# Kernel optimization log

Hardware: AMD Instinct MI355X
Metric: run time of the kernel (lower is better)

The kernel has to match this reference:

```python
import jax, jax.numpy as jnp
import numpy as np

INF_SUB_NUM = -9000000000000000.0
LN_EPS = 1e-5


def _layernorm(x, gamma, beta):
    mu = jnp.mean(x, axis=-1, keepdims=True)
    var = jnp.mean(jnp.square(x - mu), axis=-1, keepdims=True)
    return gamma * (x - mu) * jax.lax.rsqrt(var + LN_EPS) + beta


def setup_inputs() -> dict:
    key = jax.random.key(0)
    kh, ke, kt, kw1, kw2 = jax.random.split(key, 5)
    B, N, E, D = 8, 4096, 2048, 256
    stdv = 1.0 / np.sqrt(D)
    return {
        "hidden": jax.random.normal(kh, (B, N, D), dtype=jnp.float32),
        "ht": jax.random.randint(kt, (B, E, N), 0, 2, dtype=jnp.int32),
        "edge_emb": jax.random.normal(ke, (B, E, D), dtype=jnp.float32),
        "wnk": jax.random.uniform(kw1, (D, D), jnp.float32, -stdv, stdv),
        "wek": jax.random.uniform(kw2, (D, D), jnp.float32, -stdv, stdv),
        "ln_gamma": jnp.ones((D,), jnp.float32),
        "ln_beta": jnp.zeros((D,), jnp.float32),
    }


def reference(hidden, ht, edge_emb, wnk, wek, ln_gamma, ln_beta):
    # hidden: [B,N,D]; ht: [B,E,N] incidence; edge_emb: [B,E,D]
    D = hidden.shape[-1]
    scale = 1.0 / jnp.sqrt(jnp.float32(D))

    edge_emb = _layernorm(edge_emb, ln_gamma, ln_beta)          # [B,E,D]
    node_k = hidden @ wnk                                        # [B,N,D]

    # Stage 1: edges attend over their incident nodes (softmax over N, dim=2)
    edge_scores = jnp.einsum('bed,bnd->ben', edge_emb, node_k) * scale
    edge_scores = jnp.where(ht > 0, edge_scores, INF_SUB_NUM)
    attn_edge = jax.nn.softmax(edge_scores, axis=2)              # [B,E,N]
    edge_h = jnp.einsum('ben,bnd->bed', attn_edge, hidden) + edge_emb

    # Stage 2: nodes gather from edges; softmax over N (dim=1), as in source
    edge_k = edge_h @ wek                                        # [B,E,D]
    node_scores = jnp.einsum('bnd,bed->bne', node_k, edge_k) * scale
    node_scores = jnp.where(jnp.transpose(ht, (0, 2, 1)) > 0, node_scores, INF_SUB_NUM)
    attn_node = jax.nn.softmax(node_scores, axis=1)              # [B,N,E]
    node_hidden = jnp.einsum('bne,bed->bnd', attn_node, edge_h)  # [B,N,D]
    return node_hidden
```

## Files before the change

### kernel.cpp

```cpp
#include <hip/hip_runtime.h>
#include <hip/hip_bf16.h>
#include <stdint.h>


#define B_ 8
#define N_ 4096
#define E_ 2048
#define D_ 256

typedef short bf16x8 __attribute__((ext_vector_type(8)));
typedef float f32x4 __attribute__((ext_vector_type(4)));
typedef unsigned short us8 __attribute__((ext_vector_type(8)));

#define AS1 __attribute__((address_space(1)))
#define AS3 __attribute__((address_space(3)))

__device__ __forceinline__ unsigned short f2bf(float f) {
    union { float f; unsigned int u; } v; v.f = f;
    unsigned int r = v.u + 0x7fffu + ((v.u >> 16) & 1u);
    return (unsigned short)(r >> 16);
}
__device__ __forceinline__ float bf2f(unsigned short h) {
    union { unsigned int u; float f; } v; v.u = ((unsigned int)h) << 16;
    return v.f;
}
__device__ __forceinline__ float waveReduceSum(float v) {
#pragma unroll
    for (int o = 32; o > 0; o >>= 1) v += __shfl_xor(v, o, 64);
    return v;
}

__global__ __launch_bounds__(256) void ln_kernel(const float* __restrict__ x,
                                                 const float* __restrict__ gamma,
                                                 const float* __restrict__ beta,
                                                 unsigned short* __restrict__ yb) {
    __shared__ float red[8];
    const int row = blockIdx.x;
    const int t = threadIdx.x;
    const int lane = t & 63, wid = t >> 6;
    const float v = x[(size_t)row * D_ + t];
    float s = waveReduceSum(v);
    if (lane == 0) red[wid] = s;
    __syncthreads();
    const float mu = (red[0] + red[1] + red[2] + red[3]) * (1.0f / D_);
    const float d = v - mu;
    float s2 = waveReduceSum(d * d);
    if (lane == 0) red[4 + wid] = s2;
    __syncthreads();
    const float var = (red[4] + red[5] + red[6] + red[7]) * (1.0f / D_);
    yb[(size_t)row * D_ + t] = f2bf(gamma[t] * d * rsqrtf(var + 1e-5f) + beta[t]);
}

__global__ __launch_bounds__(256) void pack_mask(const int* __restrict__ ht,
                                                 uint32_t* __restrict__ bits) {
    __shared__ __align__(8) unsigned char nib[256];
    const int row = blockIdx.x;
    const int t = threadIdx.x;
    const int* hrow = ht + (size_t)row * N_;
    uint32_t* brow = bits + (size_t)row * (N_ / 32);
#pragma unroll
    for (int it = 0; it < 4; ++it) {
        const int4 v = *(const int4*)&hrow[it * 1024 + t * 4];
        unsigned char n = (unsigned char)((v.x > 0) | ((v.y > 0) << 1) |
                                          ((v.z > 0) << 2) | ((v.w > 0) << 3));
        nib[t] = n;
        __syncthreads();
        if (t < 32) {
            uint64_t x = *(const uint64_t*)&nib[t * 8];
            x = (x | (x >> 4)) & 0x00FF00FF00FF00FFull;
            x = (x | (x >> 8)) & 0x0000FFFF0000FFFFull;
            brow[it * 32 + t] = (uint32_t)(x | (x >> 16));
        }
        __syncthreads();
    }
}

__global__ __launch_bounds__(256) void prep_hidden(const float* __restrict__ in,
                                                   unsigned short* __restrict__ hb,
                                                   unsigned short* __restrict__ hT) {
    __shared__ unsigned short tile[64][65];
    const int b = blockIdx.z;
    in += (size_t)b * N_ * D_;
    hb += (size_t)b * N_ * D_;
    hT += (size_t)b * D_ * N_;
    const int n0 = blockIdx.y * 64, d0 = blockIdx.x * 64;
    const int t = threadIdx.x;
    const int tr = t >> 4, tc = (t & 15) * 4;
#pragma unroll
    for (int q = 0; q < 4; ++q) {
        const int rr = q * 16 + tr;
        const float4 f = *(const float4*)&in[(size_t)(n0 + rr) * D_ + d0 + tc];
        unsigned short h0 = f2bf(f.x), h1 = f2bf(f.y), h2 = f2bf(f.z), h3 = f2bf(f.w);
        *(ushort4*)&hb[(size_t)(n0 + rr) * D_ + d0 + tc] = make_ushort4(h0, h1, h2, h3);
        tile[rr][tc + 0] = h0; tile[rr][tc + 1] = h1;
        tile[rr][tc + 2] = h2; tile[rr][tc + 3] = h3;
    }
    __syncthreads();
#pragma unroll
    for (int q = 0; q < 4; ++q) {
        const int cc = q * 16 + tr;
        ushort4 o = make_ushort4(tile[tc + 0][cc], tile[tc + 1][cc],
                                 tile[tc + 2][cc], tile[tc + 3][cc]);
        *(ushort4*)&hT[(size_t)(d0 + cc) * N_ + n0 + tc] = o;
    }
}

__global__ __launch_bounds__(256) void cast_wT(const float* __restrict__ w,
                                               unsigned short* __restrict__ wT) {
    const int gid = blockIdx.x * 256 + threadIdx.x;
    const int i = gid >> 8, j = gid & 255;
    wT[j * D_ + i] = f2bf(w[i * D_ + j]);
}

__global__ __launch_bounds__(256) void scale_ehT(const float* __restrict__ ehT,
                                                 const float* __restrict__ lsum,
                                                 unsigned short* __restrict__ ehs) {
    const size_t base = ((size_t)blockIdx.x * 256 + threadIdx.x) * 8;
    const int b = (int)(base / ((size_t)D_ * E_));
    const int e = (int)(base % E_);
    const float4 f0 = *(const float4*)&ehT[base];
    const float4 f1 = *(const float4*)&ehT[base + 4];
    const float4 l0 = *(const float4*)&lsum[(size_t)b * E_ + e];
    const float4 l1 = *(const float4*)&lsum[(size_t)b * E_ + e + 4];
    us8 o;
    o[0] = f2bf(f0.x / l0.x); o[1] = f2bf(f0.y / l0.y);
    o[2] = f2bf(f0.z / l0.z); o[3] = f2bf(f0.w / l0.w);
    o[4] = f2bf(f1.x / l1.x); o[5] = f2bf(f1.y / l1.y);
    o[6] = f2bf(f1.z / l1.z); o[7] = f2bf(f1.w / l1.w);
    *(us8*)&ehs[base] = o;
}

__global__ __launch_bounds__(256) void gemm_bf16(const short* __restrict__ A,
                                                 const short* __restrict__ Bm,
                                                 unsigned short* __restrict__ C) {
    __shared__ __align__(16) short ls[16896];
    short* lsA = ls;
    short* lsB = ls + 8192;
    const int m0 = blockIdx.y * 128, n0 = blockIdx.x * 128;
    const int tid = threadIdx.x, wid = tid >> 6, lane = tid & 63;
    const int l15 = lane & 15, kg = lane >> 4;
    const int wr = wid >> 1, wc = wid & 1;

    int raoff[4], rota[4], rboff[4], rotb[4];
#pragma unroll
    for (int i = 0; i < 4; ++i) {
        const int ra = wr * 64 + i * 16 + l15;
        raoff[i] = ra * 64; rota[i] = kg + (ra >> 1);
        const int rb = wc * 64 + i * 16 + l15;
        rboff[i] = rb * 64; rotb[i] = kg + (rb >> 1);
    }
    const f32x4 zero = {0.f, 0.f, 0.f, 0.f};
    f32x4 acc[4][4];
#pragma unroll
    for (int i = 0; i < 4; ++i)
#pragma unroll
        for (int j = 0; j < 4; ++j) acc[i][j] = zero;

    for (int kt = 0; kt < 256; kt += 64) {
        __syncthreads();
#pragma unroll
        for (int q = 0; q < 4; ++q) {
            const int c = q * 256 + tid;
            const int r = c >> 3;
            const int kc = ((c & 7) - (r >> 1)) & 7;
            const short* ga = A + (size_t)(m0 + r) * 256 + kt + kc * 8;
            __builtin_amdgcn_global_load_lds((const AS1 void*)ga,
                (AS3 void*)(lsA + (q * 256 + wid * 64) * 8), 16, 0, 0);
            const short* gb = Bm + (size_t)(n0 + r) * 256 + kt + kc * 8;
            __builtin_amdgcn_global_load_lds((const AS1 void*)gb,
                (AS3 void*)(lsB + (q * 256 + wid * 64) * 8), 16, 0, 0);
        }
        __syncthreads();
#pragma unroll
        for (int s = 0; s < 2; ++s) {
            bf16x8 fa[4], fb[4];
#pragma unroll
            for (int i = 0; i < 4; ++i)
                fa[i] = *(const bf16x8*)(lsA + raoff[i] + (((s * 4 + rota[i]) & 7) << 3));
#pragma unroll
            for (int j = 0; j < 4; ++j)
                fb[j] = *(const bf16x8*)(lsB + rboff[j] + (((s * 4 + rotb[j]) & 7) << 3));
#pragma unroll
            for (int i = 0; i < 4; ++i)
#pragma unroll
                for (int j = 0; j < 4; ++j)
                    acc[i][j] = __builtin_amdgcn_mfma_f32_16x16x32_bf16(fa[i], fb[j], acc[i][j], 0, 0, 0);
        }
    }
    __syncthreads();
#pragma unroll
    for (int i = 0; i < 4; ++i)
#pragma unroll
        for (int r = 0; r < 4; ++r) {
            const int rowfull = wr * 64 + i * 16 + kg * 4 + r;
#pragma unroll
            for (int j = 0; j < 4; ++j) {
                const int cl = wc * 64 + j * 16 + l15;
                ls[rowfull * 132 + cl] = (short)f2bf(acc[i][j][r]);
            }
        }
    __syncthreads();
#pragma unroll
    for (int si = 0; si < 8; ++si) {
        const int row = (tid >> 4) + si * 16;
        const int col = (tid & 15) * 8;
        us8 val = *(us8*)&ls[row * 132 + col];
        *(us8*)&C[(size_t)(m0 + row) * D_ + n0 + col] = val;
    }
}

template <int MODE>
__global__ __launch_bounds__(256, 1) void fused_attn(
        const short* __restrict__ A, const short* __restrict__ B1,
        const short* __restrict__ B2, const uint32_t* __restrict__ bits,
        const unsigned short* __restrict__ eln,
        void* __restrict__ out1, float* __restrict__ out2,
        int KN, float scale) {
    __shared__ __align__(16) short ls[(MODE == 0) ? 33024 : 69888];
    const int b = blockIdx.x;
    const int m0 = blockIdx.y * 64;
    const int MA = (MODE == 2) ? N_ : E_;
    const short* Ab = A + (size_t)b * MA * D_;
    const short* B1b = B1 + (size_t)b * KN * D_;
    const short* B2b = (MODE != 0) ? (B2 + (size_t)b * D_ * KN) : nullptr;
    const uint32_t* bb = bits + (size_t)b * E_ * (N_ / 32);

    const int tid = threadIdx.x, wid = tid >> 6, lane = tid & 63;
    const int l15 = lane & 15, kg = lane >> 4;
    const int wv = wid >> 1, ww = wid & 1;

    bf16x8 fa[2][8];
#pragma unroll
    for (int mf = 0; mf < 2; ++mf) {
        const size_t ar = (size_t)(m0 + wv * 32 + mf * 16 + l15) * D_;
#pragma unroll
        for (int kf = 0; kf < 8; ++kf)
            fa[mf][kf] = *(const bf16x8*)(Ab + ar + (kf * 4 + kg) * 8);
    }

    const f32x4 zero = {0.f, 0.f, 0.f, 0.f};
    f32x4 acco[2][8];
    if (MODE != 0) {
#pragma unroll
        for (int mf = 0; mf < 2; ++mf)
#pragma unroll
            for (int jf = 0; jf < 8; ++jf) acco[mf][jf] = zero;
    }
    float rs[2][4] = {{0.f, 0.f, 0.f, 0.f}, {0.f, 0.f, 0.f, 0.f}};

    short* Pp = ls + 65536;
    const int NT = KN / 64;

#define STAGE_T(db, tt) do {                                                   \
        const int kt_ = (tt) * 64;                                             \
        short* b1d_ = ls + (db) * 16384;                                       \
        _Pragma("unroll")                                                      \
        for (int q = 0; q < 8; ++q) {                                          \
            const int c_ = q * 256 + tid;                                      \
            const int r_ = c_ >> 5;                                            \
            const int ck_ = (c_ & 31) ^ (r_ & 31);                             \
            __builtin_amdgcn_global_load_lds(                                  \
                (const AS1 void*)(B1b + (size_t)(kt_ + r_) * D_ + ck_ * 8),    \
                (AS3 void*)(b1d_ + (q * 256 + wid * 64) * 8), 16, 0, 0);       \
        }                                                                      \
        if (MODE != 0) {                                                       \
            short* b2d_ = ls + 32768 + (db) * 16384;                           \
            _Pragma("unroll")                                                  \
            for (int q = 0; q < 8; ++q) {                                      \
                const int c_ = q * 256 + tid;                                  \
                const int r_ = c_ >> 3;                                        \
                const int ck_ = (c_ & 7) ^ ((r_ >> 1) & 7);                    \
                __builtin_amdgcn_global_load_lds(                              \
                    (const AS1 void*)(B2b + (size_t)r_ * KN + kt_ + ck_ * 8),  \
                    (AS3 void*)(b2d_ + (q * 256 + wid * 64) * 8), 16, 0, 0);   \
            }                                                                  \
        }                                                                      \
    } while (0)

    STAGE_T(0, 0);
    __syncthreads();

    int cur = 0;
    for (int t = 0; t < NT; ++t) {
        if (t + 1 < NT) STAGE_T(cur ^ 1, t + 1);
        const short* b1c = ls + cur * 16384;
        f32x4 accs[2][2];
        accs[0][0] = zero; accs[0][1] = zero; accs[1][0] = zero; accs[1][1] = zero;
        const int rb0 = ww * 32 + l15, rb1 = ww * 32 + 16 + l15;
        const int x0 = kg ^ (rb0 & 31), x1 = kg ^ (rb1 & 31);
#pragma unroll
        for (int kf = 0; kf < 8; ++kf) {
            const bf16x8 fb0 = *(const bf16x8*)(b1c + rb0 * 256 + ((kf * 4) ^ x0) * 8);
            const bf16x8 fb1 = *(const bf16x8*)(b1c + rb1 * 256 + ((kf * 4) ^ x1) * 8);
            accs[0][0] = __builtin_amdgcn_mfma_f32_16x16x32_bf16(fa[0][kf], fb0, accs[0][0], 0, 0, 0);
            accs[1][0] = __builtin_amdgcn_mfma_f32_16x16x32_bf16(fa[1][kf], fb0, accs[1][0], 0, 0, 0);
            accs[0][1] = __builtin_amdgcn_mfma_f32_16x16x32_bf16(fa[0][kf], fb1, accs[0][1], 0, 0, 0);
            accs[1][1] = __builtin_amdgcn_mfma_f32_16x16x32_bf16(fa[1][kf], fb1, accs[1][1], 0, 0, 0);
        }
        const int kt0 = t * 64;
        uint64_t mw[2][4];
        uint32_t cw[2];
        if (MODE <= 1) {
#pragma unroll
            for (int mf = 0; mf < 2; ++mf)
#pragma unroll
                for (int r = 0; r < 4; ++r) {
                    const int row = m0 + wv * 32 + mf * 16 + kg * 4 + r;
                    mw[mf][r] = *(const uint64_t*)&bb[(size_t)row * (N_ / 32) + (kt0 >> 5)];
                }
        } else {
#pragma unroll
            for (int jf = 0; jf < 2; ++jf) {
                const int col = kt0 + ww * 32 + jf * 16 + l15;
                cw[jf] = bb[(size_t)col * (N_ / 32) + ((m0 + wv * 32) >> 5)];
            }
        }
#pragma unroll
        for (int mf = 0; mf < 2; ++mf)
#pragma unroll
            for (int jf = 0; jf < 2; ++jf)
#pragma unroll
                for (int r = 0; r < 4; ++r) {
                    float v = accs[mf][jf][r] * scale;
                    uint32_t bit;
                    if (MODE <= 1)
                        bit = (uint32_t)(mw[mf][r] >> (ww * 32 + jf * 16 + l15)) & 1u;
                    else
                        bit = (cw[jf] >> (mf * 16 + kg * 4 + r)) & 1u;
                    v = bit ? __expf(v) : 0.f;
                    if (MODE <= 1) rs[mf][r] += v;
                    if (MODE != 0) {
                        const int prow = wv * 32 + mf * 16 + kg * 4 + r;
                        const int pcol = ww * 32 + jf * 16 + l15;
                        Pp[prow * 64 + (((pcol >> 3) ^ ((prow >> 1) & 7)) * 8) + (pcol & 7)] =
                            (short)f2bf(v);
                    }
                }
        if (MODE != 0) {
            __syncthreads();
            const short* b2c = ls + 32768 + cur * 16384;
            const int pr0 = wv * 32 + l15, pr1 = wv * 32 + 16 + l15;
            const int px0 = kg ^ ((pr0 >> 1) & 7), px1 = kg ^ ((pr1 >> 1) & 7);
#pragma unroll
            for (int kf2 = 0; kf2 < 2; ++kf2) {
                const bf16x8 pa0 = *(const bf16x8*)(Pp + pr0 * 64 + ((kf2 * 4) ^ px0) * 8);
                const bf16x8 pa1 = *(const bf16x8*)(Pp + pr1 * 64 + ((kf2 * 4) ^ px1) * 8);
#pragma unroll
                for (int jf = 0; jf < 8; ++jf) {
                    const int rh = ww * 128 + jf * 16 + l15;
                    const bf16x8 fbh = *(const bf16x8*)(b2c + rh * 64 +
                        (((kf2 * 4 + kg) ^ ((rh >> 1) & 7))) * 8);
                    acco[0][jf] = __builtin_amdgcn_mfma_f32_16x16x32_bf16(pa0, fbh, acco[0][jf], 0, 0, 0);
                    acco[1][jf] = __builtin_amdgcn_mfma_f32_16x16x32_bf16(pa1, fbh, acco[1][jf], 0, 0, 0);
                }
            }
        }
        __syncthreads();
        cur ^= 1;
    }
#undef STAGE_T

    if (MODE == 0) {
        float* rsx = (float*)(ls + 32768);
#pragma unroll
        for (int mf = 0; mf < 2; ++mf)
#pragma unroll
            for (int r = 0; r < 4; ++r) {
                float s = rs[mf][r];
                s += __shfl_xor(s, 1, 64); s += __shfl_xor(s, 2, 64);
                s += __shfl_xor(s, 4, 64); s += __shfl_xor(s, 8, 64);
                if (l15 == 0) rsx[ww * 64 + wv * 32 + mf * 16 + kg * 4 + r] = s;
            }
        __syncthreads();
        if (tid < 64)
            ((float*)out1)[(size_t)b * E_ + m0 + tid] = rsx[tid] + rsx[64 + tid];
    } else if (MODE == 1) {
        float* rsx = (float*)(ls + 69632);
#pragma unroll
        for (int mf = 0; mf < 2; ++mf)
#pragma unroll
            for (int r = 0; r < 4; ++r) {
                float s = rs[mf][r];
                s += __shfl_xor(s, 1, 64); s += __shfl_xor(s, 2, 64);
                s += __shfl_xor(s, 4, 64); s += __shfl_xor(s, 8, 64);
                if (l15 == 0) rsx[ww * 64 + wv * 32 + mf * 16 + kg * 4 + r] = s;
            }
        __syncthreads();
        float* lsF = (float*)ls;
#pragma unroll
        for (int mf = 0; mf < 2; ++mf)
#pragma unroll
            for (int r = 0; r < 4; ++r) {
                const int row = wv * 32 + mf * 16 + kg * 4 + r;
                const float inv = 1.0f / (rsx[row] + rsx[64 + row]);
#pragma unroll
                for (int jf = 0; jf < 8; ++jf)
                    lsF[row * 261 + ww * 128 + jf * 16 + l15] = acco[mf][jf][r] * inv;
            }
        __syncthreads();
        unsigned short* ehb = (unsigned short*)out1 + (size_t)b * E_ * D_;
        const unsigned short* elnb = eln + (size_t)b * E_ * D_;
#pragma unroll
        for (int p = 0; p < 8; ++p) {
            const int idx = p * 2048 + tid * 8;
            const int row = idx >> 8, col = idx & 255;
            const us8 ev = *(const us8*)&elnb[(size_t)(m0 + row) * D_ + col];
            us8 o;
            float vv[8];
#pragma unroll
            for (int u = 0; u < 8; ++u) {
                vv[u] = lsF[row * 261 + col + u] + bf2f(ev[u]);
                o[u] = f2bf(vv[u]);
            }
            *(us8*)&ehb[(size_t)(m0 + row) * D_ + col] = o;
#pragma unroll
            for (int u = 0; u < 8; ++u)
                lsF[row * 261 + col + u] = vv[u];
        }
        __syncthreads();
        float* ehT = out2 + (size_t)b * D_ * E_;
#pragma unroll
        for (int p = 0; p < 8; ++p) {
            const int idx = p * 2048 + tid * 8;
            const int d = idx >> 6, e8 = idx & 63;
            float4 v0, v1;
            v0.x = lsF[(e8 + 0) * 261 + d]; v0.y = lsF[(e8 + 1) * 261 + d];
            v0.z = lsF[(e8 + 2) * 261 + d]; v0.w = lsF[(e8 + 3) * 261 + d];
            v1.x = lsF[(e8 + 4) * 261 + d]; v1.y = lsF[(e8 + 5) * 261 + d];
            v1.z = lsF[(e8 + 6) * 261 + d]; v1.w = lsF[(e8 + 7) * 261 + d];
            *(float4*)&ehT[(size_t)d * E_ + m0 + e8] = v0;
            *(float4*)&ehT[(size_t)d * E_ + m0 + e8 + 4] = v1;
        }
    } else {
        float* lsF = (float*)ls;
#pragma unroll
        for (int mf = 0; mf < 2; ++mf)
#pragma unroll
            for (int r = 0; r < 4; ++r) {
                const int row = wv * 32 + mf * 16 + kg * 4 + r;
#pragma unroll
                for (int jf = 0; jf < 8; ++jf)
                    lsF[row * 256 + ww * 128 + jf * 16 + l15] = acco[mf][jf][r];
            }
        __syncthreads();
        float* ob = (float*)out1 + (size_t)b * N_ * D_;
#pragma unroll
        for (int p = 0; p < 16; ++p) {
            const int lin = p * 256 + tid;
            const int row = lin >> 6, c4 = (lin & 63) * 4;
            *(float4*)&ob[(size_t)(m0 + row) * D_ + c4] = *(const float4*)&lsF[row * 256 + c4];
        }
    }
}

extern "C" void kernel_launch(void* const* d_in, const int* in_sizes, int n_in,
                              void* d_out, int out_size, void* d_ws, size_t ws_size,
                              hipStream_t stream) {
    const float* hidden = (const float*)d_in[0];
    const int* ht = (const int*)d_in[1];
    const float* edge_emb = (const float*)d_in[2];
    const float* wnk = (const float*)d_in[3];
    const float* wek = (const float*)d_in[4];
    const float* gamma = (const float*)d_in[5];
    const float* beta = (const float*)d_in[6];
    float* out = (float*)d_out;
    (void)in_sizes; (void)n_in; (void)out_size; (void)ws_size;

    char* w = (char*)d_ws;
    unsigned short* hidden_bf = (unsigned short*)w;  w += (size_t)B_ * N_ * D_ * 2;
    unsigned short* hiddenT_bf = (unsigned short*)w; w += (size_t)B_ * D_ * N_ * 2;
    unsigned short* node_k_bf = (unsigned short*)w;  w += (size_t)B_ * N_ * D_ * 2;
    unsigned short* eln_bf = (unsigned short*)w;     w += (size_t)B_ * E_ * D_ * 2;
    unsigned short* edge_h_bf = (unsigned short*)w;  w += (size_t)B_ * E_ * D_ * 2;
    float* ehT_f32 = (float*)w;                      w += (size_t)B_ * D_ * E_ * 4;
    unsigned short* ehsT_bf = (unsigned short*)w;    w += (size_t)B_ * D_ * E_ * 2;
    unsigned short* edge_k_bf = (unsigned short*)w;  w += (size_t)B_ * E_ * D_ * 2;
    uint32_t* bits = (uint32_t*)w;                   w += (size_t)B_ * E_ * (N_ / 32) * 4;
    float* lsum = (float*)w;                         w += (size_t)B_ * E_ * 4;
    unsigned short* wnkT = (unsigned short*)w;       w += (size_t)D_ * D_ * 2;
    unsigned short* wekT = (unsigned short*)w;       w += (size_t)D_ * D_ * 2;

    const float scale = 0.0625f;

    prep_hidden<<<dim3(D_ / 64, N_ / 64, B_), 256, 0, stream>>>(hidden, hidden_bf, hiddenT_bf);
    cast_wT<<<D_ * D_ / 256, 256, 0, stream>>>(wnk, wnkT);
    cast_wT<<<D_ * D_ / 256, 256, 0, stream>>>(wek, wekT);
    ln_kernel<<<B_ * E_, 256, 0, stream>>>(edge_emb, gamma, beta, eln_bf);
    pack_mask<<<B_ * E_, 256, 0, stream>>>(ht, bits);

    gemm_bf16<<<dim3(D_ / 128, (B_ * N_) / 128), 256, 0, stream>>>(
        (const short*)hidden_bf, (const short*)wnkT, node_k_bf);
    fused_attn<1><<<dim3(8, E_ / 64), 256, 0, stream>>>(
        (const short*)eln_bf, (const short*)node_k_bf, (const short*)hiddenT_bf,
        bits, eln_bf, edge_h_bf, ehT_f32, N_, scale);
    gemm_bf16<<<dim3(D_ / 128, (B_ * E_) / 128), 256, 0, stream>>>(
        (const short*)edge_h_bf, (const short*)wekT, edge_k_bf);
    fused_attn<0><<<dim3(8, E_ / 64), 256, 0, stream>>>(
        (const short*)edge_k_bf, (const short*)node_k_bf, nullptr,
        bits, nullptr, lsum, nullptr, N_, scale);
    scale_ehT<<<(B_ * D_ * E_) / (256 * 8), 256, 0, stream>>>(ehT_f32, lsum, ehsT_bf);
    fused_attn<2><<<dim3(8, N_ / 64), 256, 0, stream>>>(
        (const short*)node_k_bf, (const short*)edge_k_bf, (const short*)ehsT_bf,
        bits, nullptr, out, nullptr, E_, scale);
}
```

Before: 894.6 us.

## Halve fused attention row tile and drop double buffering for two blocks per CU

The fused attention kernels now process 32 rows per block instead of 64, with four waves each owning a 16-column slice. The double-buffered LDS staging is replaced by a single buffer loaded every iteration and followed by a barrier. This cuts LDS and registers roughly in half so two blocks fit per CU, and the grid doubles. In exchange, each loaded K/V tile is reused across half as many rows, so global and L2 traffic doubles, and the overlap between copy and compute inside a block is lost.

```diff
diff --git a/kernel.cpp b/kernel.cpp
--- a/kernel.cpp
+++ b/kernel.cpp
@@ -210,15 +210,15 @@
 }
 
 template <int MODE>
-__global__ __launch_bounds__(256, 1) void fused_attn(
+__global__ __launch_bounds__(256, 2) void fused_attn(
         const short* __restrict__ A, const short* __restrict__ B1,
         const short* __restrict__ B2, const uint32_t* __restrict__ bits,
         const unsigned short* __restrict__ eln,
         void* __restrict__ out1, float* __restrict__ out2,
         int KN, float scale) {
-    __shared__ __align__(16) short ls[(MODE == 0) ? 33024 : 69888];
+    __shared__ __align__(16) short ls[(MODE == 0) ? 16640 : 35072];
     const int b = blockIdx.x;
-    const int m0 = blockIdx.y * 64;
+    const int m0 = blockIdx.y * 32;
     const int MA = (MODE == 2) ? N_ : E_;
     const short* Ab = A + (size_t)b * MA * D_;
     const short* B1b = B1 + (size_t)b * KN * D_;
@@ -227,127 +227,112 @@
 
     const int tid = threadIdx.x, wid = tid >> 6, lane = tid & 63;
     const int l15 = lane & 15, kg = lane >> 4;
-    const int wv = wid >> 1, ww = wid & 1;
+    const int ww = wid;
 
     bf16x8 fa[2][8];
 #pragma unroll
     for (int mf = 0; mf < 2; ++mf) {
-        const size_t ar = (size_t)(m0 + wv * 32 + mf * 16 + l15) * D_;
+        const size_t ar = (size_t)(m0 + mf * 16 + l15) * D_;
 #pragma unroll
         for (int kf = 0; kf < 8; ++kf)
             fa[mf][kf] = *(const bf16x8*)(Ab + ar + (kf * 4 + kg) * 8);
     }
 
     const f32x4 zero = {0.f, 0.f, 0.f, 0.f};
-    f32x4 acco[2][8];
+    f32x4 acco[2][4];
     if (MODE != 0) {
 #pragma unroll
         for (int mf = 0; mf < 2; ++mf)
 #pragma unroll
-            for (int jf = 0; jf < 8; ++jf) acco[mf][jf] = zero;
+            for (int jf = 0; jf < 4; ++jf) acco[mf][jf] = zero;
     }
     float rs[2][4] = {{0.f, 0.f, 0.f, 0.f}, {0.f, 0.f, 0.f, 0.f}};
 
-    short* Pp = ls + 65536;
+    short* Pp = ls + 32768;
     const int NT = KN / 64;
 
-#define STAGE_T(db, tt) do {                                                   \
-        const int kt_ = (tt) * 64;                                             \
-        short* b1d_ = ls + (db) * 16384;                                       \
-        _Pragma("unroll")                                                      \
-        for (int q = 0; q < 8; ++q) {                                          \
-            const int c_ = q * 256 + tid;                                      \
-            const int r_ = c_ >> 5;                                            \
-            const int ck_ = (c_ & 31) ^ (r_ & 31);                             \
-            __builtin_amdgcn_global_load_lds(                                  \
-                (const AS1 void*)(B1b + (size_t)(kt_ + r_) * D_ + ck_ * 8),    \
-                (AS3 void*)(b1d_ + (q * 256 + wid * 64) * 8), 16, 0, 0);       \
-        }                                                                      \
-        if (MODE != 0) {                                                       \
-            short* b2d_ = ls + 32768 + (db) * 16384;                           \
-            _Pragma("unroll")                                                  \
-            for (int q = 0; q < 8; ++q) {                                      \
-                const int c_ = q * 256 + tid;                                  \
-                const int r_ = c_ >> 3;                                        \
-                const int ck_ = (c_ & 7) ^ ((r_ >> 1) & 7);                    \
-                __builtin_amdgcn_global_load_lds(                              \
-                    (const AS1 void*)(B2b + (size_t)r_ * KN + kt_ + ck_ * 8),  \
-                    (AS3 void*)(b2d_ + (q * 256 + wid * 64) * 8), 16, 0, 0);   \
-            }                                                                  \
-        }                                                                      \
-    } while (0)
-
-    STAGE_T(0, 0);
-    __syncthreads();
-
-    int cur = 0;
     for (int t = 0; t < NT; ++t) {
-        if (t + 1 < NT) STAGE_T(cur ^ 1, t + 1);
-        const short* b1c = ls + cur * 16384;
-        f32x4 accs[2][2];
-        accs[0][0] = zero; accs[0][1] = zero; accs[1][0] = zero; accs[1][1] = zero;
-        const int rb0 = ww * 32 + l15, rb1 = ww * 32 + 16 + l15;
-        const int x0 = kg ^ (rb0 & 31), x1 = kg ^ (rb1 & 31);
+        {
+            const int kt_ = t * 64;
+#pragma unroll
+            for (int q = 0; q < 8; ++q) {
+                const int c_ = q * 256 + tid;
+                const int r_ = c_ >> 5;
+                const int ck_ = (c_ & 31) ^ (r_ & 31);
+                __builtin_amdgcn_global_load_lds(
+                    (const AS1 void*)(B1b + (size_t)(kt_ + r_) * D_ + ck_ * 8),
+                    (AS3 void*)(ls + (q * 256 + wid * 64) * 8), 16, 0, 0);
+            }
+            if (MODE != 0) {
+#pragma unroll
+                for (int q = 0; q < 8; ++q) {
+                    const int c_ = q * 256 + tid;
+                    const int r_ = c_ >> 3;
+                    const int ck_ = (c_ & 7) ^ ((r_ >> 1) & 7);
+                    __builtin_amdgcn_global_load_lds(
+                        (const AS1 void*)(B2b + (size_t)r_ * KN + kt_ + ck_ * 8),
+                        (AS3 void*)(ls + 16384 + (q * 256 + wid * 64) * 8), 16, 0, 0);
+                }
+            }
+        }
+        __syncthreads();
+
+        f32x4 accs[2];
+        accs[0] = zero; accs[1] = zero;
+        const int rb = ww * 16 + l15;
+        const int xb = kg ^ (rb & 31);
 #pragma unroll
         for (int kf = 0; kf < 8; ++kf) {
-            const bf16x8 fb0 = *(const bf16x8*)(b1c + rb0 * 256 + ((kf * 4) ^ x0) * 8);
-            const bf16x8 fb1 = *(const bf16x8*)(b1c + rb1 * 256 + ((kf * 4) ^ x1) * 8);
-            accs[0][0] = __builtin_amdgcn_mfma_f32_16x16x32_bf16(fa[0][kf], fb0, accs[0][0], 0, 0, 0);
-            accs[1][0] = __builtin_amdgcn_mfma_f32_16x16x32_bf16(fa[1][kf], fb0, accs[1][0], 0, 0, 0);
-            accs[0][1] = __builtin_amdgcn_mfma_f32_16x16x32_bf16(fa[0][kf], fb1, accs[0][1], 0, 0, 0);
-            accs[1][1] = __builtin_amdgcn_mfma_f32_16x16x32_bf16(fa[1][kf], fb1, accs[1][1], 0, 0, 0);
+            const bf16x8 fb = *(const bf16x8*)(ls + rb * 256 + ((kf * 4) ^ xb) * 8);
+            accs[0] = __builtin_amdgcn_mfma_f32_16x16x32_bf16(fa[0][kf], fb, accs[0], 0, 0, 0);
+            accs[1] = __builtin_amdgcn_mfma_f32_16x16x32_bf16(fa[1][kf], fb, accs[1], 0, 0, 0);
         }
         const int kt0 = t * 64;
         uint64_t mw[2][4];
-        uint32_t cw[2];
+        uint32_t cw;
         if (MODE <= 1) {
 #pragma unroll
             for (int mf = 0; mf < 2; ++mf)
 #pragma unroll
                 for (int r = 0; r < 4; ++r) {
-                    const int row = m0 + wv * 32 + mf * 16 + kg * 4 + r;
+                    const int row = m0 + mf * 16 + kg * 4 + r;
                     mw[mf][r] = *(const uint64_t*)&bb[(size_t)row * (N_ / 32) + (kt0 >> 5)];
                 }
         } else {
-#pragma unroll
-            for (int jf = 0; jf < 2; ++jf) {
-                const int col = kt0 + ww * 32 + jf * 16 + l15;
-                cw[jf] = bb[(size_t)col * (N_ / 32) + ((m0 + wv * 32) >> 5)];
-            }
-        }
-#pragma unroll
-        for (int mf = 0; mf < 2; ++mf)
-#pragma unroll
-            for (int jf = 0; jf < 2; ++jf)
-#pragma unroll
-                for (int r = 0; r < 4; ++r) {
-                    float v = accs[mf][jf][r] * scale;
-                    uint32_t bit;
-                    if (MODE <= 1)
-                        bit = (uint32_t)(mw[mf][r] >> (ww * 32 + jf * 16 + l15)) & 1u;
-                    else
-                        bit = (cw[jf] >> (mf * 16 + kg * 4 + r)) & 1u;
-                    v = bit ? __expf(v) : 0.f;
-                    if (MODE <= 1) rs[mf][r] += v;
-                    if (MODE != 0) {
-                        const int prow = wv * 32 + mf * 16 + kg * 4 + r;
-                        const int pcol = ww * 32 + jf * 16 + l15;
-                        Pp[prow * 64 + (((pcol >> 3) ^ ((prow >> 1) & 7)) * 8) + (pcol & 7)] =
-                            (short)f2bf(v);
-                    }
+            const int col = kt0 + ww * 16 + l15;
+            cw = bb[(size_t)col * (N_ / 32) + (m0 >> 5)];
+        }
+#pragma unroll
+        for (int mf = 0; mf < 2; ++mf)
+#pragma unroll
+            for (int r = 0; r < 4; ++r) {
+                float v = accs[mf][r] * scale;
+                uint32_t bit;
+                if (MODE <= 1)
+                    bit = (uint32_t)(mw[mf][r] >> (ww * 16 + l15)) & 1u;
+                else
+                    bit = (cw >> (mf * 16 + kg * 4 + r)) & 1u;
+                v = bit ? __expf(v) : 0.f;
+                if (MODE <= 1) rs[mf][r] += v;
+                if (MODE != 0) {
+                    const int prow = mf * 16 + kg * 4 + r;
+                    const int pcol = ww * 16 + l15;
+                    Pp[prow * 64 + (((pcol >> 3) ^ ((prow >> 1) & 7)) * 8) + (pcol & 7)] =
+                        (short)f2bf(v);
                 }
+            }
         if (MODE != 0) {
             __syncthreads();
-            const short* b2c = ls + 32768 + cur * 16384;
-            const int pr0 = wv * 32 + l15, pr1 = wv * 32 + 16 + l15;
+            const short* b2c = ls + 16384;
+            const int pr0 = l15, pr1 = 16 + l15;
             const int px0 = kg ^ ((pr0 >> 1) & 7), px1 = kg ^ ((pr1 >> 1) & 7);
 #pragma unroll
             for (int kf2 = 0; kf2 < 2; ++kf2) {
-                const bf16x8 pa0 = *(const bf16x8*)(Pp + pr0 * 64 + ((kf2 * 4) ^ px0) * 8);
-                const bf16x8 pa1 = *(const bf16x8*)(Pp + pr1 * 64 + ((kf2 * 4) ^ px1) * 8);
-#pragma unroll
-                for (int jf = 0; jf < 8; ++jf) {
-                    const int rh = ww * 128 + jf * 16 + l15;
+                const bf16x8 pa0 = *(const bf16x8*)(Pp + pr0 * 64 + (((kf2 * 4) ^ px0)) * 8);
+                const bf16x8 pa1 = *(const bf16x8*)(Pp + pr1 * 64 + (((kf2 * 4) ^ px1)) * 8);
+#pragma unroll
+                for (int jf = 0; jf < 4; ++jf) {
+                    const int rh = ww * 64 + jf * 16 + l15;
                     const bf16x8 fbh = *(const bf16x8*)(b2c + rh * 64 +
                         (((kf2 * 4 + kg) ^ ((rh >> 1) & 7))) * 8);
                     acco[0][jf] = __builtin_amdgcn_mfma_f32_16x16x32_bf16(pa0, fbh, acco[0][jf], 0, 0, 0);
@@ -356,12 +341,10 @@
             }
         }
         __syncthreads();
-        cur ^= 1;
-    }
-#undef STAGE_T
+    }
 
     if (MODE == 0) {
-        float* rsx = (float*)(ls + 32768);
+        float* rsx = (float*)(ls + 16384);
 #pragma unroll
         for (int mf = 0; mf < 2; ++mf)
 #pragma unroll
@@ -369,13 +352,14 @@
                 float s = rs[mf][r];
                 s += __shfl_xor(s, 1, 64); s += __shfl_xor(s, 2, 64);
                 s += __shfl_xor(s, 4, 64); s += __shfl_xor(s, 8, 64);
-                if (l15 == 0) rsx[ww * 64 + wv * 32 + mf * 16 + kg * 4 + r] = s;
-            }
-        __syncthreads();
-        if (tid < 64)
-            ((float*)out1)[(size_t)b * E_ + m0 + tid] = rsx[tid] + rsx[64 + tid];
+                if (l15 == 0) rsx[ww * 32 + mf * 16 + kg * 4 + r] = s;
+            }
+        __syncthreads();
+        if (tid < 32)
+            ((float*)out1)[(size_t)b * E_ + m0 + tid] =
+                rsx[tid] + rsx[32 + tid] + rsx[64 + tid] + rsx[96 + tid];
     } else if (MODE == 1) {
-        float* rsx = (float*)(ls + 69632);
+        float* rsx = (float*)(ls + 34816);
 #pragma unroll
         for (int mf = 0; mf < 2; ++mf)
 #pragma unroll
@@ -383,7 +367,7 @@
                 float s = rs[mf][r];
                 s += __shfl_xor(s, 1, 64); s += __shfl_xor(s, 2, 64);
                 s += __shfl_xor(s, 4, 64); s += __shfl_xor(s, 8, 64);
-                if (l15 == 0) rsx[ww * 64 + wv * 32 + mf * 16 + kg * 4 + r] = s;
+                if (l15 == 0) rsx[ww * 32 + mf * 16 + kg * 4 + r] = s;
             }
         __syncthreads();
         float* lsF = (float*)ls;
@@ -391,17 +375,18 @@
         for (int mf = 0; mf < 2; ++mf)
 #pragma unroll
             for (int r = 0; r < 4; ++r) {
-                const int row = wv * 32 + mf * 16 + kg * 4 + r;
-                const float inv = 1.0f / (rsx[row] + rsx[64 + row]);
-#pragma unroll
-                for (int jf = 0; jf < 8; ++jf)
-                    lsF[row * 261 + ww * 128 + jf * 16 + l15] = acco[mf][jf][r] * inv;
+                const int row = mf * 16 + kg * 4 + r;
+                const float inv = 1.0f /
+                    (rsx[row] + rsx[32 + row] + rsx[64 + row] + rsx[96 + row]);
+#pragma unroll
+                for (int jf = 0; jf < 4; ++jf)
+                    lsF[row * 261 + ww * 64 + jf * 16 + l15] = acco[mf][jf][r] * inv;
             }
         __syncthreads();
         unsigned short* ehb = (unsigned short*)out1 + (size_t)b * E_ * D_;
         const unsigned short* elnb = eln + (size_t)b * E_ * D_;
 #pragma unroll
-        for (int p = 0; p < 8; ++p) {
+        for (int p = 0; p < 4; ++p) {
             const int idx = p * 2048 + tid * 8;
             const int row = idx >> 8, col = idx & 255;
             const us8 ev = *(const us8*)&elnb[(size_t)(m0 + row) * D_ + col];
@@ -420,9 +405,9 @@
         __syncthreads();
         float* ehT = out2 + (size_t)b * D_ * E_;
 #pragma unroll
-        for (int p = 0; p < 8; ++p) {
+        for (int p = 0; p < 4; ++p) {
             const int idx = p * 2048 + tid * 8;
-            const int d = idx >> 6, e8 = idx & 63;
+            const int d = idx >> 5, e8 = idx & 31;
             float4 v0, v1;
             v0.x = lsF[(e8 + 0) * 261 + d]; v0.y = lsF[(e8 + 1) * 261 + d];
             v0.z = lsF[(e8 + 2) * 261 + d]; v0.w = lsF[(e8 + 3) * 261 + d];
@@ -437,15 +422,15 @@
         for (int mf = 0; mf < 2; ++mf)
 #pragma unroll
             for (int r = 0; r < 4; ++r) {
-                const int row = wv * 32 + mf * 16 + kg * 4 + r;
-#pragma unroll
-                for (int jf = 0; jf < 8; ++jf)
-                    lsF[row * 256 + ww * 128 + jf * 16 + l15] = acco[mf][jf][r];
+                const int row = mf * 16 + kg * 4 + r;
+#pragma unroll
+                for (int jf = 0; jf < 4; ++jf)
+                    lsF[row * 256 + ww * 64 + jf * 16 + l15] = acco[mf][jf][r];
             }
         __syncthreads();
         float* ob = (float*)out1 + (size_t)b * N_ * D_;
 #pragma unroll
-        for (int p = 0; p < 16; ++p) {
+        for (int p = 0; p < 8; ++p) {
             const int lin = p * 256 + tid;
             const int row = lin >> 6, c4 = (lin & 63) * 4;
             *(float4*)&ob[(size_t)(m0 + row) * D_ + c4] = *(const float4*)&lsF[row * 256 + c4];
@@ -490,16 +475,16 @@
 
     gemm_bf16<<<dim3(D_ / 128, (B_ * N_) / 128), 256, 0, stream>>>(
         (const short*)hidden_bf, (const short*)wnkT, node_k_bf);
-    fused_attn<1><<<dim3(8, E_ / 64), 256, 0, stream>>>(
+    fused_attn<1><<<dim3(8, E_ / 32), 256, 0, stream>>>(
         (const short*)eln_bf, (const short*)node_k_bf, (const short*)hiddenT_bf,
         bits, eln_bf, edge_h_bf, ehT_f32, N_, scale);
     gemm_bf16<<<dim3(D_ / 128, (B_ * E_) / 128), 256, 0, stream>>>(
         (const short*)edge_h_bf, (const short*)wekT, edge_k_bf);
-    fused_attn<0><<<dim3(8, E_ / 64), 256, 0, stream>>>(
+    fused_attn<0><<<dim3(8, E_ / 32), 256, 0, stream>>>(
         (const short*)edge_k_bf, (const short*)node_k_bf, nullptr,
         bits, nullptr, lsum, nullptr, N_, scale);
     scale_ehT<<<(B_ * D_ * E_) / (256 * 8), 256, 0, stream>>>(ehT_f32, lsum, ehsT_bf);
-    fused_attn<2><<<dim3(8, N_ / 64), 256, 0, stream>>>(
+    fused_attn<2><<<dim3(8, N_ / 32), 256, 0, stream>>>(
         (const short*)node_k_bf, (const short*)edge_k_bf, (const short*)ehsT_bf,
         bits, nullptr, out, nullptr, E_, scale);
 }
```

New measurement: 843.5 us. -5.7%, faster.

## Split edge attention over N, shrink LDS for two blocks per CU, add reduction kernel

Applied to the files above, without the earlier changes.

Stage-1 attention now splits the N dimension into two halves via a z grid dimension. Each half writes unnormalized partial outputs and partial row sums to fp32 slabs, and a new reduce_pv kernel combines them, normalizes, adds the layernorm residual, and writes both the bf16 and transposed fp32 edge_h. The fused attention kernels drop double buffering of B2/B1 in modes 1 and 2 to cut LDS, and launch bounds allow 2 blocks per CU. Mode 0 uses 32-row tiles to double its grid. The aim is more occupancy and more blocks for the small grids, at the cost of extra slab traffic, an extra launch, and less load/compute overlap within a block.

```diff
diff --git a/kernel.cpp b/kernel.cpp
--- a/kernel.cpp
+++ b/kernel.cpp
@@ -110,6 +110,46 @@
     const int gid = blockIdx.x * 256 + threadIdx.x;
     const int i = gid >> 8, j = gid & 255;
     wT[j * D_ + i] = f2bf(w[i * D_ + j]);
+}
+
+__global__ __launch_bounds__(256) void reduce_pv(const float* __restrict__ slab,
+                                                 const unsigned short* __restrict__ eln,
+                                                 const float* __restrict__ rsump,
+                                                 unsigned short* __restrict__ eh,
+                                                 float* __restrict__ ehT) {
+    __shared__ float tile[64][65];
+    const int b = blockIdx.z;
+    const float* s0 = slab + (size_t)b * E_ * D_;
+    const float* s1 = slab + (size_t)(B_ + b) * E_ * D_;
+    const int e0 = blockIdx.y * 64, d0 = blockIdx.x * 64;
+    const int t = threadIdx.x;
+    const int tr = t >> 4, tc = (t & 15) * 4;
+#pragma unroll
+    for (int q = 0; q < 4; ++q) {
+        const int rr = q * 16 + tr;
+        const int row = e0 + rr;
+        const float4 v0 = *(const float4*)&s0[(size_t)row * D_ + d0 + tc];
+        const float4 v1 = *(const float4*)&s1[(size_t)row * D_ + d0 + tc];
+        const float inv = 1.0f / (rsump[(size_t)b * E_ + row] +
+                                  rsump[(size_t)B_ * E_ + (size_t)b * E_ + row]);
+        const ushort4 el = *(const ushort4*)&eln[(size_t)b * E_ * D_ + (size_t)row * D_ + d0 + tc];
+        const float x0 = (v0.x + v1.x) * inv + bf2f(el.x);
+        const float x1 = (v0.y + v1.y) * inv + bf2f(el.y);
+        const float x2 = (v0.z + v1.z) * inv + bf2f(el.z);
+        const float x3 = (v0.w + v1.w) * inv + bf2f(el.w);
+        *(ushort4*)&eh[(size_t)b * E_ * D_ + (size_t)row * D_ + d0 + tc] =
+            make_ushort4(f2bf(x0), f2bf(x1), f2bf(x2), f2bf(x3));
+        tile[rr][tc + 0] = x0; tile[rr][tc + 1] = x1;
+        tile[rr][tc + 2] = x2; tile[rr][tc + 3] = x3;
+    }
+    __syncthreads();
+#pragma unroll
+    for (int q = 0; q < 4; ++q) {
+        const int cc = q * 16 + tr;
+        float4 o = make_float4(tile[tc + 0][cc], tile[tc + 1][cc],
+                               tile[tc + 2][cc], tile[tc + 3][cc]);
+        *(float4*)&ehT[(size_t)b * D_ * E_ + (size_t)(d0 + cc) * E_ + e0 + tc] = o;
+    }
 }
 
 __global__ __launch_bounds__(256) void scale_ehT(const float* __restrict__ ehT,
@@ -210,15 +250,14 @@
 }
 
 template <int MODE>
-__global__ __launch_bounds__(256, 1) void fused_attn(
+__global__ __launch_bounds__(256, 2) void fused_attn(
         const short* __restrict__ A, const short* __restrict__ B1,
         const short* __restrict__ B2, const uint32_t* __restrict__ bits,
-        const unsigned short* __restrict__ eln,
-        void* __restrict__ out1, float* __restrict__ out2,
+        void* __restrict__ out1, float* __restrict__ sums,
         int KN, float scale) {
-    __shared__ __align__(16) short ls[(MODE == 0) ? 33024 : 69888];
+    __shared__ __align__(16) short ls[(MODE == 0) ? 33024 : ((MODE == 1) ? 37120 : 36864)];
     const int b = blockIdx.x;
-    const int m0 = blockIdx.y * 64;
+    const int m0 = blockIdx.y * ((MODE == 0) ? 32 : 64);
     const int MA = (MODE == 2) ? N_ : E_;
     const short* Ab = A + (size_t)b * MA * D_;
     const short* B1b = B1 + (size_t)b * KN * D_;
@@ -227,12 +266,18 @@
 
     const int tid = threadIdx.x, wid = tid >> 6, lane = tid & 63;
     const int l15 = lane & 15, kg = lane >> 4;
-    const int wv = wid >> 1, ww = wid & 1;
+    const int wv = wid >> 1, ww2 = wid & 1;
+    const int ww4 = wid;
+
+    const int kbase = (MODE == 1) ? blockIdx.z * (KN >> 1) : 0;
+    const int NT = ((MODE == 1) ? (KN >> 1) : KN) / 64;
 
     bf16x8 fa[2][8];
 #pragma unroll
     for (int mf = 0; mf < 2; ++mf) {
-        const size_t ar = (size_t)(m0 + wv * 32 + mf * 16 + l15) * D_;
+        const int arow = (MODE == 0) ? (m0 + mf * 16 + l15)
+                                     : (m0 + wv * 32 + mf * 16 + l15);
+        const size_t ar = (size_t)arow * D_;
 #pragma unroll
         for (int kf = 0; kf < 8; ++kf)
             fa[mf][kf] = *(const bf16x8*)(Ab + ar + (kf * 4 + kg) * 8);
@@ -248,12 +293,10 @@
     }
     float rs[2][4] = {{0.f, 0.f, 0.f, 0.f}, {0.f, 0.f, 0.f, 0.f}};
 
-    short* Pp = ls + 65536;
-    const int NT = KN / 64;
-
-#define STAGE_T(db, tt) do {                                                   \
-        const int kt_ = (tt) * 64;                                             \
-        short* b1d_ = ls + (db) * 16384;                                       \
+    short* Pp = ls + 32768;
+
+#define STAGE_B1(base_, tt) do {                                               \
+        const int kt_ = kbase + (tt) * 64;                                     \
         _Pragma("unroll")                                                      \
         for (int q = 0; q < 8; ++q) {                                          \
             const int c_ = q * 256 + tid;                                      \
@@ -261,84 +304,114 @@
             const int ck_ = (c_ & 31) ^ (r_ & 31);                             \
             __builtin_amdgcn_global_load_lds(                                  \
                 (const AS1 void*)(B1b + (size_t)(kt_ + r_) * D_ + ck_ * 8),    \
-                (AS3 void*)(b1d_ + (q * 256 + wid * 64) * 8), 16, 0, 0);       \
-        }                                                                      \
-        if (MODE != 0) {                                                       \
-            short* b2d_ = ls + 32768 + (db) * 16384;                           \
-            _Pragma("unroll")                                                  \
-            for (int q = 0; q < 8; ++q) {                                      \
-                const int c_ = q * 256 + tid;                                  \
-                const int r_ = c_ >> 3;                                        \
-                const int ck_ = (c_ & 7) ^ ((r_ >> 1) & 7);                    \
-                __builtin_amdgcn_global_load_lds(                              \
-                    (const AS1 void*)(B2b + (size_t)r_ * KN + kt_ + ck_ * 8),  \
-                    (AS3 void*)(b2d_ + (q * 256 + wid * 64) * 8), 16, 0, 0);   \
-            }                                                                  \
+                (AS3 void*)((base_) + (q * 256 + wid * 64) * 8), 16, 0, 0);    \
         }                                                                      \
     } while (0)
 
-    STAGE_T(0, 0);
-    __syncthreads();
+#define STAGE_B2(tt) do {                                                      \
+        const int kt_ = kbase + (tt) * 64;                                     \
+        _Pragma("unroll")                                                      \
+        for (int q = 0; q < 8; ++q) {                                          \
+            const int c_ = q * 256 + tid;                                      \
+            const int r_ = c_ >> 3;                                            \
+            const int ck_ = (c_ & 7) ^ ((r_ >> 1) & 7);                        \
+            __builtin_amdgcn_global_load_lds(                                  \
+                (const AS1 void*)(B2b + (size_t)r_ * KN + kt_ + ck_ * 8),      \
+                (AS3 void*)(ls + 16384 + (q * 256 + wid * 64) * 8), 16, 0, 0); \
+        }                                                                      \
+    } while (0)
 
     int cur = 0;
+    STAGE_B1(ls, 0);
+    if (MODE != 0) STAGE_B2(0);
+    __syncthreads();
+
     for (int t = 0; t < NT; ++t) {
-        if (t + 1 < NT) STAGE_T(cur ^ 1, t + 1);
-        const short* b1c = ls + cur * 16384;
-        f32x4 accs[2][2];
-        accs[0][0] = zero; accs[0][1] = zero; accs[1][0] = zero; accs[1][1] = zero;
-        const int rb0 = ww * 32 + l15, rb1 = ww * 32 + 16 + l15;
-        const int x0 = kg ^ (rb0 & 31), x1 = kg ^ (rb1 & 31);
-#pragma unroll
-        for (int kf = 0; kf < 8; ++kf) {
-            const bf16x8 fb0 = *(const bf16x8*)(b1c + rb0 * 256 + ((kf * 4) ^ x0) * 8);
-            const bf16x8 fb1 = *(const bf16x8*)(b1c + rb1 * 256 + ((kf * 4) ^ x1) * 8);
-            accs[0][0] = __builtin_amdgcn_mfma_f32_16x16x32_bf16(fa[0][kf], fb0, accs[0][0], 0, 0, 0);
-            accs[1][0] = __builtin_amdgcn_mfma_f32_16x16x32_bf16(fa[1][kf], fb0, accs[1][0], 0, 0, 0);
-            accs[0][1] = __builtin_amdgcn_mfma_f32_16x16x32_bf16(fa[0][kf], fb1, accs[0][1], 0, 0, 0);
-            accs[1][1] = __builtin_amdgcn_mfma_f32_16x16x32_bf16(fa[1][kf], fb1, accs[1][1], 0, 0, 0);
-        }
-        const int kt0 = t * 64;
-        uint64_t mw[2][4];
-        uint32_t cw[2];
-        if (MODE <= 1) {
+        const int kt0 = kbase + t * 64;
+        if (MODE == 0) {
+            if (t + 1 < NT) STAGE_B1(ls + (cur ^ 1) * 16384, t + 1);
+            const short* b1c = ls + cur * 16384;
+            f32x4 accs[2];
+            accs[0] = zero; accs[1] = zero;
+            const int rb = ww4 * 16 + l15;
+            const int xb = kg ^ (rb & 31);
+#pragma unroll
+            for (int kf = 0; kf < 8; ++kf) {
+                const bf16x8 fb = *(const bf16x8*)(b1c + rb * 256 + ((kf * 4) ^ xb) * 8);
+                accs[0] = __builtin_amdgcn_mfma_f32_16x16x32_bf16(fa[0][kf], fb, accs[0], 0, 0, 0);
+                accs[1] = __builtin_amdgcn_mfma_f32_16x16x32_bf16(fa[1][kf], fb, accs[1], 0, 0, 0);
+            }
+            uint64_t mw[2][4];
 #pragma unroll
             for (int mf = 0; mf < 2; ++mf)
 #pragma unroll
                 for (int r = 0; r < 4; ++r) {
-                    const int row = m0 + wv * 32 + mf * 16 + kg * 4 + r;
+                    const int row = m0 + mf * 16 + kg * 4 + r;
                     mw[mf][r] = *(const uint64_t*)&bb[(size_t)row * (N_ / 32) + (kt0 >> 5)];
                 }
+#pragma unroll
+            for (int mf = 0; mf < 2; ++mf)
+#pragma unroll
+                for (int r = 0; r < 4; ++r) {
+                    float v = accs[mf][r] * scale;
+                    const uint32_t bit = (uint32_t)(mw[mf][r] >> (ww4 * 16 + l15)) & 1u;
+                    rs[mf][r] += bit ? __expf(v) : 0.f;
+                }
+            __syncthreads();
+            cur ^= 1;
         } else {
-#pragma unroll
-            for (int jf = 0; jf < 2; ++jf) {
-                const int col = kt0 + ww * 32 + jf * 16 + l15;
-                cw[jf] = bb[(size_t)col * (N_ / 32) + ((m0 + wv * 32) >> 5)];
-            }
-        }
-#pragma unroll
-        for (int mf = 0; mf < 2; ++mf)
-#pragma unroll
-            for (int jf = 0; jf < 2; ++jf)
-#pragma unroll
-                for (int r = 0; r < 4; ++r) {
-                    float v = accs[mf][jf][r] * scale;
-                    uint32_t bit;
-                    if (MODE <= 1)
-                        bit = (uint32_t)(mw[mf][r] >> (ww * 32 + jf * 16 + l15)) & 1u;
-                    else
-                        bit = (cw[jf] >> (mf * 16 + kg * 4 + r)) & 1u;
-                    v = bit ? __expf(v) : 0.f;
-                    if (MODE <= 1) rs[mf][r] += v;
-                    if (MODE != 0) {
+            f32x4 accs[2][2];
+            accs[0][0] = zero; accs[0][1] = zero; accs[1][0] = zero; accs[1][1] = zero;
+            const int rb0 = ww2 * 32 + l15, rb1 = ww2 * 32 + 16 + l15;
+            const int x0 = kg ^ (rb0 & 31), x1 = kg ^ (rb1 & 31);
+#pragma unroll
+            for (int kf = 0; kf < 8; ++kf) {
+                const bf16x8 fb0 = *(const bf16x8*)(ls + rb0 * 256 + ((kf * 4) ^ x0) * 8);
+                const bf16x8 fb1 = *(const bf16x8*)(ls + rb1 * 256 + ((kf * 4) ^ x1) * 8);
+                accs[0][0] = __builtin_amdgcn_mfma_f32_16x16x32_bf16(fa[0][kf], fb0, accs[0][0], 0, 0, 0);
+                accs[1][0] = __builtin_amdgcn_mfma_f32_16x16x32_bf16(fa[1][kf], fb0, accs[1][0], 0, 0, 0);
+                accs[0][1] = __builtin_amdgcn_mfma_f32_16x16x32_bf16(fa[0][kf], fb1, accs[0][1], 0, 0, 0);
+                accs[1][1] = __builtin_amdgcn_mfma_f32_16x16x32_bf16(fa[1][kf], fb1, accs[1][1], 0, 0, 0);
+            }
+            uint64_t mw[2][4];
+            uint32_t cw[2];
+            if (MODE == 1) {
+#pragma unroll
+                for (int mf = 0; mf < 2; ++mf)
+#pragma unroll
+                    for (int r = 0; r < 4; ++r) {
+                        const int row = m0 + wv * 32 + mf * 16 + kg * 4 + r;
+                        mw[mf][r] = *(const uint64_t*)&bb[(size_t)row * (N_ / 32) + (kt0 >> 5)];
+                    }
+            } else {
+#pragma unroll
+                for (int jf = 0; jf < 2; ++jf) {
+                    const int col = kt0 + ww2 * 32 + jf * 16 + l15;
+                    cw[jf] = bb[(size_t)col * (N_ / 32) + ((m0 + wv * 32) >> 5)];
+                }
+            }
+#pragma unroll
+            for (int mf = 0; mf < 2; ++mf)
+#pragma unroll
+                for (int jf = 0; jf < 2; ++jf)
+#pragma unroll
+                    for (int r = 0; r < 4; ++r) {
+                        float v = accs[mf][jf][r] * scale;
+                        uint32_t bit;
+                        if (MODE == 1)
+                            bit = (uint32_t)(mw[mf][r] >> (ww2 * 32 + jf * 16 + l15)) & 1u;
+                        else
+                            bit = (cw[jf] >> (mf * 16 + kg * 4 + r)) & 1u;
+                        v = bit ? __expf(v) : 0.f;
+                        if (MODE == 1) rs[mf][r] += v;
                         const int prow = wv * 32 + mf * 16 + kg * 4 + r;
-                        const int pcol = ww * 32 + jf * 16 + l15;
+                        const int pcol = ww2 * 32 + jf * 16 + l15;
                         Pp[prow * 64 + (((pcol >> 3) ^ ((prow >> 1) & 7)) * 8) + (pcol & 7)] =
                             (short)f2bf(v);
                     }
-                }
-        if (MODE != 0) {
             __syncthreads();
-            const short* b2c = ls + 32768 + cur * 16384;
+            if (t + 1 < NT) STAGE_B1(ls, t + 1);
+            const short* b2c = ls + 16384;
             const int pr0 = wv * 32 + l15, pr1 = wv * 32 + 16 + l15;
             const int px0 = kg ^ ((pr0 >> 1) & 7), px1 = kg ^ ((pr1 >> 1) & 7);
 #pragma unroll
@@ -347,18 +420,19 @@
                 const bf16x8 pa1 = *(const bf16x8*)(Pp + pr1 * 64 + ((kf2 * 4) ^ px1) * 8);
 #pragma unroll
                 for (int jf = 0; jf < 8; ++jf) {
-                    const int rh = ww * 128 + jf * 16 + l15;
+                    const int rh = ww2 * 128 + jf * 16 + l15;
                     const bf16x8 fbh = *(const bf16x8*)(b2c + rh * 64 +
                         (((kf2 * 4 + kg) ^ ((rh >> 1) & 7))) * 8);
                     acco[0][jf] = __builtin_amdgcn_mfma_f32_16x16x32_bf16(pa0, fbh, acco[0][jf], 0, 0, 0);
                     acco[1][jf] = __builtin_amdgcn_mfma_f32_16x16x32_bf16(pa1, fbh, acco[1][jf], 0, 0, 0);
                 }
             }
-        }
-        __syncthreads();
-        cur ^= 1;
-    }
-#undef STAGE_T
+            __syncthreads();
+            if (t + 1 < NT) STAGE_B2(t + 1);
+        }
+    }
+#undef STAGE_B1
+#undef STAGE_B2
 
     if (MODE == 0) {
         float* rsx = (float*)(ls + 32768);
@@ -369,13 +443,14 @@
                 float s = rs[mf][r];
                 s += __shfl_xor(s, 1, 64); s += __shfl_xor(s, 2, 64);
                 s += __shfl_xor(s, 4, 64); s += __shfl_xor(s, 8, 64);
-                if (l15 == 0) rsx[ww * 64 + wv * 32 + mf * 16 + kg * 4 + r] = s;
-            }
-        __syncthreads();
-        if (tid < 64)
-            ((float*)out1)[(size_t)b * E_ + m0 + tid] = rsx[tid] + rsx[64 + tid];
+                if (l15 == 0) rsx[ww4 * 32 + mf * 16 + kg * 4 + r] = s;
+            }
+        __syncthreads();
+        if (tid < 32)
+            sums[(size_t)b * E_ + m0 + tid] =
+                rsx[tid] + rsx[32 + tid] + rsx[64 + tid] + rsx[96 + tid];
     } else if (MODE == 1) {
-        float* rsx = (float*)(ls + 69632);
+        float* rsx = (float*)(ls + 36864);
 #pragma unroll
         for (int mf = 0; mf < 2; ++mf)
 #pragma unroll
@@ -383,53 +458,30 @@
                 float s = rs[mf][r];
                 s += __shfl_xor(s, 1, 64); s += __shfl_xor(s, 2, 64);
                 s += __shfl_xor(s, 4, 64); s += __shfl_xor(s, 8, 64);
-                if (l15 == 0) rsx[ww * 64 + wv * 32 + mf * 16 + kg * 4 + r] = s;
-            }
-        __syncthreads();
+                if (l15 == 0) rsx[ww2 * 64 + wv * 32 + mf * 16 + kg * 4 + r] = s;
+            }
+        __syncthreads();
+        if (tid < 64)
+            sums[(size_t)blockIdx.z * B_ * E_ + (size_t)b * E_ + m0 + tid] =
+                rsx[tid] + rsx[64 + tid];
         float* lsF = (float*)ls;
 #pragma unroll
         for (int mf = 0; mf < 2; ++mf)
 #pragma unroll
             for (int r = 0; r < 4; ++r) {
                 const int row = wv * 32 + mf * 16 + kg * 4 + r;
-                const float inv = 1.0f / (rsx[row] + rsx[64 + row]);
 #pragma unroll
                 for (int jf = 0; jf < 8; ++jf)
-                    lsF[row * 261 + ww * 128 + jf * 16 + l15] = acco[mf][jf][r] * inv;
-            }
-        __syncthreads();
-        unsigned short* ehb = (unsigned short*)out1 + (size_t)b * E_ * D_;
-        const unsigned short* elnb = eln + (size_t)b * E_ * D_;
-#pragma unroll
-        for (int p = 0; p < 8; ++p) {
-            const int idx = p * 2048 + tid * 8;
-            const int row = idx >> 8, col = idx & 255;
-            const us8 ev = *(const us8*)&elnb[(size_t)(m0 + row) * D_ + col];
-            us8 o;
-            float vv[8];
-#pragma unroll
-            for (int u = 0; u < 8; ++u) {
-                vv[u] = lsF[row * 261 + col + u] + bf2f(ev[u]);
-                o[u] = f2bf(vv[u]);
-            }
-            *(us8*)&ehb[(size_t)(m0 + row) * D_ + col] = o;
-#pragma unroll
-            for (int u = 0; u < 8; ++u)
-                lsF[row * 261 + col + u] = vv[u];
-        }
-        __syncthreads();
-        float* ehT = out2 + (size_t)b * D_ * E_;
-#pragma unroll
-        for (int p = 0; p < 8; ++p) {
-            const int idx = p * 2048 + tid * 8;
-            const int d = idx >> 6, e8 = idx & 63;
-            float4 v0, v1;
-            v0.x = lsF[(e8 + 0) * 261 + d]; v0.y = lsF[(e8 + 1) * 261 + d];
-            v0.z = lsF[(e8 + 2) * 261 + d]; v0.w = lsF[(e8 + 3) * 261 + d];
-            v1.x = lsF[(e8 + 4) * 261 + d]; v1.y = lsF[(e8 + 5) * 261 + d];
-            v1.z = lsF[(e8 + 6) * 261 + d]; v1.w = lsF[(e8 + 7) * 261 + d];
-            *(float4*)&ehT[(size_t)d * E_ + m0 + e8] = v0;
-            *(float4*)&ehT[(size_t)d * E_ + m0 + e8 + 4] = v1;
+                    lsF[row * 256 + ww2 * 128 + jf * 16 + l15] = acco[mf][jf][r];
+            }
+        __syncthreads();
+        float* sl = (float*)out1 + ((size_t)blockIdx.z * B_ + b) * (size_t)E_ * D_ +
+                    (size_t)m0 * D_;
+#pragma unroll
+        for (int p = 0; p < 16; ++p) {
+            const int lin = p * 256 + tid;
+            const int row = lin >> 6, c4 = (lin & 63) * 4;
+            *(float4*)&sl[(size_t)row * D_ + c4] = *(const float4*)&lsF[row * 256 + c4];
         }
     } else {
         float* lsF = (float*)ls;
@@ -440,7 +492,7 @@
                 const int row = wv * 32 + mf * 16 + kg * 4 + r;
 #pragma unroll
                 for (int jf = 0; jf < 8; ++jf)
-                    lsF[row * 256 + ww * 128 + jf * 16 + l15] = acco[mf][jf][r];
+                    lsF[row * 256 + ww2 * 128 + jf * 16 + l15] = acco[mf][jf][r];
             }
         __syncthreads();
         float* ob = (float*)out1 + (size_t)b * N_ * D_;
@@ -475,6 +527,8 @@
     float* ehT_f32 = (float*)w;                      w += (size_t)B_ * D_ * E_ * 4;
     unsigned short* ehsT_bf = (unsigned short*)w;    w += (size_t)B_ * D_ * E_ * 2;
     unsigned short* edge_k_bf = (unsigned short*)w;  w += (size_t)B_ * E_ * D_ * 2;
+    float* slabs = (float*)w;                        w += (size_t)2 * B_ * E_ * D_ * 4;
+    float* rsump = (float*)w;                        w += (size_t)2 * B_ * E_ * 4;
     uint32_t* bits = (uint32_t*)w;                   w += (size_t)B_ * E_ * (N_ / 32) * 4;
     float* lsum = (float*)w;                         w += (size_t)B_ * E_ * 4;
     unsigned short* wnkT = (unsigned short*)w;       w += (size_t)D_ * D_ * 2;
@@ -490,16 +544,18 @@
 
     gemm_bf16<<<dim3(D_ / 128, (B_ * N_) / 128), 256, 0, stream>>>(
         (const short*)hidden_bf, (const short*)wnkT, node_k_bf);
-    fused_attn<1><<<dim3(8, E_ / 64), 256, 0, stream>>>(
+    fused_attn<1><<<dim3(8, E_ / 64, 2), 256, 0, stream>>>(
         (const short*)eln_bf, (const short*)node_k_bf, (const short*)hiddenT_bf,
-        bits, eln_bf, edge_h_bf, ehT_f32, N_, scale);
+        bits, slabs, rsump, N_, scale);
+    reduce_pv<<<dim3(D_ / 64, E_ / 64, B_), 256, 0, stream>>>(
+        slabs, eln_bf, rsump, edge_h_bf, ehT_f32);
     gemm_bf16<<<dim3(D_ / 128, (B_ * E_) / 128), 256, 0, stream>>>(
         (const short*)edge_h_bf, (const short*)wekT, edge_k_bf);
-    fused_attn<0><<<dim3(8, E_ / 64), 256, 0, stream>>>(
+    fused_attn<0><<<dim3(8, E_ / 32), 256, 0, stream>>>(
         (const short*)edge_k_bf, (const short*)node_k_bf, nullptr,
-        bits, nullptr, lsum, nullptr, N_, scale);
+        bits, nullptr, lsum, N_, scale);
     scale_ehT<<<(B_ * D_ * E_) / (256 * 8), 256, 0, stream>>>(ehT_f32, lsum, ehsT_bf);
     fused_attn<2><<<dim3(8, N_ / 64), 256, 0, stream>>>(
         (const short*)node_k_bf, (const short*)edge_k_bf, (const short*)ehsT_bf,
-        bits, nullptr, out, nullptr, E_, scale);
-}
+        bits, out, nullptr, E_, scale);
+}
```

New measurement: 860.8 us. 1.04x faster.
